# Kernel optimization log

Measured on AMD Instinct MI355X. Metric: run time of the kernel, lower is better.

Reference implementation:

```python
import jax, jax.numpy as jnp
import numpy as np

B, CIN, H, W = 16, 3, 112, 112
S, D, C, NC = 3, 4, 128, 100   # num_scales, depth, channels, num_classes
THRESH = 0.9
WSCALE = 0.05  # keep activations numerically sane through relu-conv cascade


def _conv3x3(x, w, b):
    # x: [B,Cin,H,W], w: [Cout,Cin,3,3]
    y = jax.lax.conv_general_dilated(
        x, w, window_strides=(1, 1), padding='SAME',
        dimension_numbers=('NCHW', 'OIHW', 'NCHW'))
    return y + b[None, :, None, None]


def setup_inputs() -> dict:
    key = jax.random.key(0)
    k = jax.random.split(key, 7)
    return {
        'x': jax.random.normal(k[0], (B, CIN, H, W), jnp.float32),
        'init_w': jax.random.normal(k[1], (S, C, CIN, 3, 3), jnp.float32) * WSCALE,
        'init_b': jax.random.normal(k[2], (S, C), jnp.float32) * WSCALE,
        'block_w': jax.random.normal(k[3], (D, S, C, C, 3, 3), jnp.float32) * WSCALE,
        'block_b': jax.random.normal(k[4], (D, S, C), jnp.float32) * WSCALE,
        'cls_w': jax.random.normal(k[5], (D, NC, C), jnp.float32) * WSCALE,
        'cls_b': jax.random.normal(k[6], (D, NC), jnp.float32) * WSCALE,
    }


def reference(x, init_w, init_b, block_w, block_b, cls_w, cls_b):
    # init blocks: one conv per scale (no activation, as in source)
    feats = [_conv3x3(x, init_w[s], init_b[s]) for s in range(S)]

    outputs = jnp.zeros((x.shape[0], cls_w.shape[1]), x.dtype)
    exited = jnp.zeros((x.shape[0],), jnp.bool_)

    # exit_layers = [0..D-1], so classifier index == block index
    for i in range(D):
        feats = [jax.nn.relu(_conv3x3(feats[s], block_w[i, s], block_b[i, s]))
                 for s in range(S)]
        pooled = feats[-1].mean(axis=(2, 3))              # [B, C]
        logits = pooled @ cls_w[i].T + cls_b[i]           # [B, NC]
        conf = jnp.max(jax.nn.softmax(logits, axis=-1), axis=-1)
        take = jnp.logical_and(~exited, conf >= THRESH)   # vectorized early-exit
        outputs = jnp.where(take[:, None], logits, outputs)
        exited = jnp.logical_or(exited, take)

    # samples that never exited get the last classifier's logits
    final_logits = feats[-1].mean(axis=(2, 3)) @ cls_w[-1].T + cls_b[-1]
    outputs = jnp.where(exited[:, None], outputs, final_logits)
    return outputs
```

## Files before the change

### kernel.cpp

```cpp
#include <hip/hip_runtime.h>
#include <hip/hip_bf16.h>


typedef unsigned int uint;
typedef unsigned short u16;
typedef __bf16 bf16x8 __attribute__((ext_vector_type(8)));
typedef short short8 __attribute__((ext_vector_type(8)));
typedef unsigned short ushort8 __attribute__((ext_vector_type(8)));
typedef float f32x4 __attribute__((ext_vector_type(4)));

#define NB   16
#define CCH  128
#define NCLS 100
#define HW   12544
#define NTILE 98

__device__ __forceinline__ u16 f2bf(float f) {
    uint u = __float_as_uint(f);
    return (u16)((u + 0x7fffu + ((u >> 16) & 1u)) >> 16);
}

__device__ __forceinline__ void gload16(const u16* g, u16* l) {
    __builtin_amdgcn_global_load_lds(
        (const __attribute__((address_space(1))) uint*)g,
        (__attribute__((address_space(3))) uint*)l, 16, 0, 0);
}

__global__ __launch_bounds__(256) void convert_w(
    const float* __restrict__ bw, u16* __restrict__ wbs)
{
    int idx = blockIdx.x * 256 + threadIdx.x;
    if (idx >= 4 * 147456) return;
    int d = idx / 147456, r = idx % 147456;
    int s = r >> 12;
    int p = r & 4095;
    int co = p >> 5, gpos = (p >> 3) & 3, e = p & 7;
    int q = s / 9, t = s % 9;
    int cin = q * 32 + ((gpos ^ ((co >> 1) & 3)) << 3) + e;
    float v = bw[(((size_t)(d * 3 + 2) * 128 + co) * 128 + cin) * 9 + t];
    wbs[idx] = f2bf(v);
}

__global__ __launch_bounds__(256) void conv_init(
    const float* __restrict__ in,
    const float* __restrict__ wgt,
    const float* __restrict__ bias,
    u16* __restrict__ outp)
{
    const int tile = blockIdx.x;
    const int cg   = blockIdx.y;
    const int n    = blockIdx.z;
    const int h0 = (tile / 7) * 16, w0 = (tile % 7) * 16;
    const int tid = threadIdx.x;
    const int sid = tid & 63, wv = tid >> 6;
    const int tx = sid & 7, ty = sid >> 3;

    __shared__ float s_in[3][18][18];
    __shared__ float s_w[3][9][32];

    float acc[2][2][8];
    #pragma unroll
    for (int a = 0; a < 2; a++)
        #pragma unroll
        for (int b = 0; b < 2; b++)
            #pragma unroll
            for (int c = 0; c < 8; c++) acc[a][b][c] = 0.f;

    const float* in_n = in + (size_t)n * 3 * HW;
    const int cbase = cg * 32;

    for (int e = tid; e < 3 * 324; e += 256) {
        int ck = e / 324, p = e % 324;
        int y = p / 18, x = p % 18;
        int gh = h0 + y - 1, gw = w0 + x - 1;
        float v = 0.f;
        if ((unsigned)gh < 112u && (unsigned)gw < 112u)
            v = in_n[(size_t)ck * HW + gh * 112 + gw];
        s_in[ck][y][x] = v;
    }
    for (int e = tid; e < 3 * 9 * 32; e += 256) {
        int co = e / 27, r = e % 27;
        int ck = r / 9, kidx = r % 9;
        s_w[ck][kidx][co] = wgt[((size_t)(cbase + co) * 3 + ck) * 9 + kidx];
    }
    __syncthreads();

    #pragma unroll
    for (int ck = 0; ck < 3; ck++) {
        float rowv[4][4];
        #pragma unroll
        for (int r = 0; r < 4; r++) {
            float2 a  = *(const float2*)&s_in[ck][ty * 2 + r][tx * 2];
            float2 b2 = *(const float2*)&s_in[ck][ty * 2 + r][tx * 2 + 2];
            rowv[r][0] = a.x; rowv[r][1] = a.y;
            rowv[r][2] = b2.x; rowv[r][3] = b2.y;
        }
        #pragma unroll
        for (int kh = 0; kh < 3; kh++)
            #pragma unroll
            for (int kw = 0; kw < 3; kw++) {
                float i00 = rowv[kh][kw],     i01 = rowv[kh][kw + 1];
                float i10 = rowv[kh + 1][kw], i11 = rowv[kh + 1][kw + 1];
                const float* wp = &s_w[ck][kh * 3 + kw][wv * 8];
                #pragma unroll
                for (int co = 0; co < 8; co++) {
                    float wval = wp[co];
                    acc[0][0][co] += i00 * wval;
                    acc[0][1][co] += i01 * wval;
                    acc[1][0][co] += i10 * wval;
                    acc[1][1][co] += i11 * wval;
                }
            }
    }

    float bv[8];
    #pragma unroll
    for (int co = 0; co < 8; co++) bv[co] = bias[cbase + wv * 8 + co];
    #pragma unroll
    for (int dy = 0; dy < 2; dy++)
        #pragma unroll
        for (int dx = 0; dx < 2; dx++) {
            ushort8 pk;
            #pragma unroll
            for (int co = 0; co < 8; co++)
                pk[co] = f2bf(acc[dy][dx][co] + bv[co]);
            int h = h0 + ty * 2 + dy, w = w0 + tx * 2 + dx;
            *(ushort8*)(outp + (((size_t)n * HW + h * 112 + w) << 7) + cbase + wv * 8) = pk;
        }
}

#define AS 40

template<bool STORE>
__global__ __launch_bounds__(256, 3) void conv_mfma(
    const u16* __restrict__ in,
    const u16* __restrict__ wbs,
    const float* __restrict__ bias,
    u16* __restrict__ outp,
    float* __restrict__ partial)
{
    __shared__ u16 s_in[180 * AS];
    __shared__ u16 s_w[4][4096];
    float* s_pool = (float*)s_in;

    const int tile = blockIdx.x;
    const int n    = blockIdx.y;
    const int h0 = (tile / 7) * 8, w0 = (tile % 7) * 16;
    const int tid = threadIdx.x, lane = tid & 63;
    const int wid = tid >> 6, wm = wid >> 1, wn = wid & 1;
    const int l15 = lane & 15, l4 = lane >> 4;

    const u16* in_n = in + ((size_t)n * HW << 7);

    const u16* wsrc_base = wbs + wid * 1024 + (lane << 3);
    u16* wdst_base = &s_w[0][0] + wid * 1024;

    #pragma unroll
    for (int s01 = 0; s01 < 2; ++s01) {
        const u16* src = wsrc_base + (s01 << 12);
        u16* dst = wdst_base + (s01 << 12);
        gload16(src, dst);
        gload16(src + 512, dst + 512);
    }

    #pragma unroll
    for (int r2 = 0; r2 < 3; ++r2) {
        int g = tid + (r2 << 8);
        if (g < 720) {
            int px = g >> 2, c8 = (g & 3) << 3;
            int hh = px / 18, ww2 = px - hh * 18;
            int gh = h0 + hh - 1, gw = w0 + ww2 - 1;
            uint4 v = make_uint4(0, 0, 0, 0);
            if ((unsigned)gh < 112u && (unsigned)gw < 112u)
                v = *(const uint4*)(in_n + ((size_t)(gh * 112 + gw) << 7) + c8);
            *(uint4*)(s_in + px * AS + c8) = v;
        }
    }

    f32x4 acc[4][4];
    #pragma unroll
    for (int i = 0; i < 4; ++i)
        #pragma unroll
        for (int j = 0; j < 4; ++j)
            #pragma unroll
            for (int e = 0; e < 4; ++e) acc[i][j][e] = 0.f;

    int a_base[4], b_base[4];
    #pragma unroll
    for (int fi = 0; fi < 4; ++fi) a_base[fi] = (wm * 4 + fi) * 18 + l15;
    #pragma unroll
    for (int nj = 0; nj < 4; ++nj)
        b_base[nj] = (wn * 64 + nj * 16 + l15) * 32 + ((l4 ^ ((l15 >> 1) & 3)) << 3);

    __syncthreads();

    #pragma unroll
    for (int P = 0; P < 18; ++P) {
        const int s0 = 2 * P, s1 = 2 * P + 1;

        #pragma unroll
        for (int d2 = 2; d2 < 4; ++d2) {
            const int sp = s0 + d2;
            if (sp < 36) {
                const u16* src = wsrc_base + (sp << 12);
                u16* dst = wdst_base + ((sp & 3) << 12);
                gload16(src, dst);
                gload16(src + 512, dst + 512);
            }
        }

        {
            const int t = s0 % 9, kh = t / 3, kw = t - kh * 3;
            bf16x8 a[4], b[4];
            #pragma unroll
            for (int fi = 0; fi < 4; ++fi) {
                const u16* p = s_in + (a_base[fi] + kh * 18 + kw) * AS + (l4 << 3);
                a[fi] = __builtin_bit_cast(bf16x8, *(const short8*)p);
            }
            const u16* rb = &s_w[s0 & 3][0];
            #pragma unroll
            for (int nj = 0; nj < 4; ++nj)
                b[nj] = __builtin_bit_cast(bf16x8, *(const short8*)(rb + b_base[nj]));
            #pragma unroll
            for (int fi = 0; fi < 4; ++fi)
                #pragma unroll
                for (int nj = 0; nj < 4; ++nj)
                    acc[fi][nj] = __builtin_amdgcn_mfma_f32_16x16x32_bf16(
                        a[fi], b[nj], acc[fi][nj], 0, 0, 0);
        }

        if (s0 % 9 == 8) {
            const int qn = s0 / 9 + 1;
            asm volatile("s_waitcnt lgkmcnt(0)" ::: "memory");
            __builtin_amdgcn_s_barrier();
            #pragma unroll
            for (int r2 = 0; r2 < 3; ++r2) {
                int g = tid + (r2 << 8);
                if (g < 720) {
                    int px = g >> 2, c8 = (g & 3) << 3;
                    int hh = px / 18, ww2 = px - hh * 18;
                    int gh = h0 + hh - 1, gw = w0 + ww2 - 1;
                    uint4 v = make_uint4(0, 0, 0, 0);
                    if ((unsigned)gh < 112u && (unsigned)gw < 112u)
                        v = *(const uint4*)(in_n + ((size_t)(gh * 112 + gw) << 7)
                                            + (qn << 5) + c8);
                    *(uint4*)(s_in + px * AS + c8) = v;
                }
            }
            asm volatile("s_waitcnt lgkmcnt(0)" ::: "memory");
            __builtin_amdgcn_s_barrier();
            __builtin_amdgcn_sched_barrier(0);
        }

        {
            const int t = s1 % 9, kh = t / 3, kw = t - kh * 3;
            bf16x8 a[4], b[4];
            #pragma unroll
            for (int fi = 0; fi < 4; ++fi) {
                const u16* p = s_in + (a_base[fi] + kh * 18 + kw) * AS + (l4 << 3);
                a[fi] = __builtin_bit_cast(bf16x8, *(const short8*)p);
            }
            const u16* rb = &s_w[s1 & 3][0];
            #pragma unroll
            for (int nj = 0; nj < 4; ++nj)
                b[nj] = __builtin_bit_cast(bf16x8, *(const short8*)(rb + b_base[nj]));
            #pragma unroll
            for (int fi = 0; fi < 4; ++fi)
                #pragma unroll
                for (int nj = 0; nj < 4; ++nj)
                    acc[fi][nj] = __builtin_amdgcn_mfma_f32_16x16x32_bf16(
                        a[fi], b[nj], acc[fi][nj], 0, 0, 0);
        }

        asm volatile("s_waitcnt vmcnt(0)" ::: "memory");
        __builtin_amdgcn_s_barrier();
        __builtin_amdgcn_sched_barrier(0);

        if (s1 % 9 == 8 && s1 != 35) {
            const int qn = s1 / 9 + 1;
            #pragma unroll
            for (int r2 = 0; r2 < 3; ++r2) {
                int g = tid + (r2 << 8);
                if (g < 720) {
                    int px = g >> 2, c8 = (g & 3) << 3;
                    int hh = px / 18, ww2 = px - hh * 18;
                    int gh = h0 + hh - 1, gw = w0 + ww2 - 1;
                    uint4 v = make_uint4(0, 0, 0, 0);
                    if ((unsigned)gh < 112u && (unsigned)gw < 112u)
                        v = *(const uint4*)(in_n + ((size_t)(gh * 112 + gw) << 7)
                                            + (qn << 5) + c8);
                    *(uint4*)(s_in + px * AS + c8) = v;
                }
            }
            asm volatile("s_waitcnt lgkmcnt(0)" ::: "memory");
            __builtin_amdgcn_s_barrier();
            __builtin_amdgcn_sched_barrier(0);
        }
    }

    float bv[4], ps[4];
    #pragma unroll
    for (int nj = 0; nj < 4; ++nj) { bv[nj] = bias[wn * 64 + nj * 16 + l15]; ps[nj] = 0.f; }
    u16* out_n = outp + ((size_t)n * HW << 7);
    #pragma unroll
    for (int fi = 0; fi < 4; ++fi) {
        int h = h0 + wm * 4 + fi;
        #pragma unroll
        for (int j = 0; j < 4; ++j) {
            int w = w0 + (l4 << 2) + j;
            u16* pr = out_n + ((size_t)(h * 112 + w) << 7);
            #pragma unroll
            for (int nj = 0; nj < 4; ++nj) {
                float v = fmaxf(acc[fi][nj][j] + bv[nj], 0.f);
                ps[nj] += v;
                if (STORE) pr[wn * 64 + nj * 16 + l15] = f2bf(v);
            }
        }
    }
    #pragma unroll
    for (int nj = 0; nj < 4; ++nj) {
        ps[nj] += __shfl_xor(ps[nj], 16, 64);
        ps[nj] += __shfl_xor(ps[nj], 32, 64);
    }
    __syncthreads();
    if (l4 == 0) {
        #pragma unroll
        for (int nj = 0; nj < 4; ++nj)
            s_pool[wm * 128 + wn * 64 + nj * 16 + l15] = ps[nj];
    }
    __syncthreads();
    if (tid < 128)
        partial[((size_t)n * NTILE + tile) * 128 + tid] = s_pool[tid] + s_pool[128 + tid];
}

__global__ __launch_bounds__(128) void logits_k(
    const float* __restrict__ partial,
    const float* __restrict__ cw,
    const float* __restrict__ cb,
    float* __restrict__ lg)
{
    const int i = blockIdx.x, n = blockIdx.y;
    const int tid = threadIdx.x;
    __shared__ float pool[128];
    const float* pp = partial + ((size_t)(i * NB + n) * NTILE) * 128;
    float s = 0.f;
    for (int t = 0; t < NTILE; ++t) s += pp[t * 128 + tid];
    pool[tid] = s * (1.f / HW);
    __syncthreads();
    if (tid < NCLS) {
        const float* wp = cw + ((size_t)i * NCLS + tid) * CCH;
        float a = cb[i * NCLS + tid];
        #pragma unroll
        for (int c = 0; c < CCH; c += 4) {
            float4 w4 = *(const float4*)(wp + c);
            a += pool[c] * w4.x + pool[c + 1] * w4.y
               + pool[c + 2] * w4.z + pool[c + 3] * w4.w;
        }
        lg[(i * NB + n) * NCLS + tid] = a;
    }
}

__global__ __launch_bounds__(256) void select_k(
    const float* __restrict__ lg,
    float* __restrict__ out)
{
    __shared__ float slg[4 * NB * NCLS];
    __shared__ int chosen[NB];
    const int tid = threadIdx.x;
    for (int e = tid; e < 4 * NB * NCLS; e += 256) slg[e] = lg[e];
    __syncthreads();
    if (tid < NB) {
        int n = tid, ch = 3;
        for (int i = 0; i < 3; i++) {
            const float* row = &slg[(i * NB + n) * NCLS];
            float m = -1e30f;
            for (int j = 0; j < NCLS; j++) m = fmaxf(m, row[j]);
            float se = 0.f;
            for (int j = 0; j < NCLS; j++) se += expf(row[j] - m);
            if (1.f / se >= 0.9f) { ch = i; break; }
        }
        chosen[n] = ch;
    }
    __syncthreads();
    for (int e = tid; e < NB * NCLS; e += 256) {
        int n = e / NCLS, j = e % NCLS;
        out[e] = slg[(chosen[n] * NB + n) * NCLS + j];
    }
}

extern "C" void kernel_launch(void* const* d_in, const int* in_sizes, int n_in,
                              void* d_out, int out_size, void* d_ws, size_t ws_size,
                              hipStream_t stream) {
    const float* x       = (const float*)d_in[0];
    const float* init_w  = (const float*)d_in[1];
    const float* init_b  = (const float*)d_in[2];
    const float* block_w = (const float*)d_in[3];
    const float* block_b = (const float*)d_in[4];
    const float* cls_w   = (const float*)d_in[5];
    const float* cls_b   = (const float*)d_in[6];
    float* out = (float*)d_out;

    char* ws = (char*)d_ws;
    u16* fA        = (u16*)ws;
    u16* fB        = (u16*)(ws + 51380224);
    u16* wbs       = (u16*)(ws + 102760448);
    float* partial = (float*)(ws + 103940096);
    float* lgbuf   = (float*)(ws + 107151360);

    convert_w<<<2304, 256, 0, stream>>>(block_w, wbs);
    conv_init<<<dim3(49, 4, NB), 256, 0, stream>>>(
        x, init_w + 2 * 128 * 27, init_b + 2 * 128, fA);

    u16* cur = fA;
    u16* nxt = fB;
    for (int i = 0; i < 4; ++i) {
        if (i < 3)
            conv_mfma<true><<<dim3(NTILE, NB), 256, 0, stream>>>(
                cur, wbs + (size_t)i * 147456, block_b + (i * 3 + 2) * 128, nxt,
                partial + (size_t)i * NB * NTILE * 128);
        else
            conv_mfma<false><<<dim3(NTILE, NB), 256, 0, stream>>>(
                cur, wbs + (size_t)i * 147456, block_b + (i * 3 + 2) * 128, nxt,
                partial + (size_t)i * NB * NTILE * 128);
        u16* t = cur; cur = nxt; nxt = t;
    }

    logits_k<<<dim3(4, NB), 128, 0, stream>>>(partial, cls_w, cls_b, lgbuf);
    select_k<<<1, 256, 0, stream>>>(lgbuf, out);
}
```

Before: 315.6 us.

## Switch weight staging to a 3-buffer ring with per-step barriers and 4 blocks/CU

Replaces the 4-slot weight ring, which was processed two K-steps per barrier, with a 3-slot ring processed one step at a time. It waits with vmcnt(2) so the prefetch two steps ahead stays in flight. The smaller LDS footprint lets launch bounds request 4 resident blocks per CU instead of 3, raising occupancy so other blocks can hide latency. The cost is twice as many barriers per block and possible register pressure from the tighter bound.

Result: faster. 297.9 us (-5.6%).

```diff
diff --git a/kernel.cpp b/kernel.cpp
--- a/kernel.cpp
+++ b/kernel.cpp
@@ -132,7 +132,7 @@
 #define AS 40
 
 template<bool STORE>
-__global__ __launch_bounds__(256, 3) void conv_mfma(
+__global__ __launch_bounds__(256, 4) void conv_mfma(
     const u16* __restrict__ in,
     const u16* __restrict__ wbs,
     const float* __restrict__ bias,
@@ -140,7 +140,7 @@
     float* __restrict__ partial)
 {
     __shared__ u16 s_in[180 * AS];
-    __shared__ u16 s_w[4][4096];
+    __shared__ u16 s_w[3][4096];
     float* s_pool = (float*)s_in;
 
     const int tile = blockIdx.x;
@@ -195,44 +195,43 @@
     __syncthreads();
 
     #pragma unroll
-    for (int P = 0; P < 18; ++P) {
-        const int s0 = 2 * P, s1 = 2 * P + 1;
-
-        #pragma unroll
-        for (int d2 = 2; d2 < 4; ++d2) {
-            const int sp = s0 + d2;
-            if (sp < 36) {
-                const u16* src = wsrc_base + (sp << 12);
-                u16* dst = wdst_base + ((sp & 3) << 12);
-                gload16(src, dst);
-                gload16(src + 512, dst + 512);
-            }
-        }
-
-        {
-            const int t = s0 % 9, kh = t / 3, kw = t - kh * 3;
-            bf16x8 a[4], b[4];
-            #pragma unroll
-            for (int fi = 0; fi < 4; ++fi) {
-                const u16* p = s_in + (a_base[fi] + kh * 18 + kw) * AS + (l4 << 3);
-                a[fi] = __builtin_bit_cast(bf16x8, *(const short8*)p);
-            }
-            const u16* rb = &s_w[s0 & 3][0];
+    for (int s = 0; s < 36; ++s) {
+        if (s + 2 < 36) {
+            const u16* src = wsrc_base + ((s + 2) << 12);
+            u16* dst = wdst_base + (((s + 2) % 3) << 12);
+            gload16(src, dst);
+            gload16(src + 512, dst + 512);
+        }
+
+        const int t = s % 9, kh = t / 3, kw = t - kh * 3;
+        bf16x8 a[4], b[4];
+        #pragma unroll
+        for (int fi = 0; fi < 4; ++fi) {
+            const u16* p = s_in + (a_base[fi] + kh * 18 + kw) * AS + (l4 << 3);
+            a[fi] = __builtin_bit_cast(bf16x8, *(const short8*)p);
+        }
+        const u16* rb = &s_w[s % 3][0];
+        #pragma unroll
+        for (int nj = 0; nj < 4; ++nj)
+            b[nj] = __builtin_bit_cast(bf16x8, *(const short8*)(rb + b_base[nj]));
+
+        #pragma unroll
+        for (int fi = 0; fi < 4; ++fi)
             #pragma unroll
             for (int nj = 0; nj < 4; ++nj)
-                b[nj] = __builtin_bit_cast(bf16x8, *(const short8*)(rb + b_base[nj]));
-            #pragma unroll
-            for (int fi = 0; fi < 4; ++fi)
-                #pragma unroll
-                for (int nj = 0; nj < 4; ++nj)
-                    acc[fi][nj] = __builtin_amdgcn_mfma_f32_16x16x32_bf16(
-                        a[fi], b[nj], acc[fi][nj], 0, 0, 0);
-        }
-
-        if (s0 % 9 == 8) {
-            const int qn = s0 / 9 + 1;
+                acc[fi][nj] = __builtin_amdgcn_mfma_f32_16x16x32_bf16(
+                    a[fi], b[nj], acc[fi][nj], 0, 0, 0);
+
+        if (s < 35) {
+            if (s + 2 < 36) asm volatile("s_waitcnt vmcnt(2)" ::: "memory");
+            else            asm volatile("s_waitcnt vmcnt(0)" ::: "memory");
             asm volatile("s_waitcnt lgkmcnt(0)" ::: "memory");
             __builtin_amdgcn_s_barrier();
+            __builtin_amdgcn_sched_barrier(0);
+        }
+
+        if (t == 8 && s < 35) {
+            const int qn = s / 9 + 1;
             #pragma unroll
             for (int r2 = 0; r2 < 3; ++r2) {
                 int g = tid + (r2 << 8);
@@ -251,51 +250,6 @@
             __builtin_amdgcn_s_barrier();
             __builtin_amdgcn_sched_barrier(0);
         }
-
-        {
-            const int t = s1 % 9, kh = t / 3, kw = t - kh * 3;
-            bf16x8 a[4], b[4];
-            #pragma unroll
-            for (int fi = 0; fi < 4; ++fi) {
-                const u16* p = s_in + (a_base[fi] + kh * 18 + kw) * AS + (l4 << 3);
-                a[fi] = __builtin_bit_cast(bf16x8, *(const short8*)p);
-            }
-            const u16* rb = &s_w[s1 & 3][0];
-            #pragma unroll
-            for (int nj = 0; nj < 4; ++nj)
-                b[nj] = __builtin_bit_cast(bf16x8, *(const short8*)(rb + b_base[nj]));
-            #pragma unroll
-            for (int fi = 0; fi < 4; ++fi)
-                #pragma unroll
-                for (int nj = 0; nj < 4; ++nj)
-                    acc[fi][nj] = __builtin_amdgcn_mfma_f32_16x16x32_bf16(
-                        a[fi], b[nj], acc[fi][nj], 0, 0, 0);
-        }
-
-        asm volatile("s_waitcnt vmcnt(0)" ::: "memory");
-        __builtin_amdgcn_s_barrier();
-        __builtin_amdgcn_sched_barrier(0);
-
-        if (s1 % 9 == 8 && s1 != 35) {
-            const int qn = s1 / 9 + 1;
-            #pragma unroll
-            for (int r2 = 0; r2 < 3; ++r2) {
-                int g = tid + (r2 << 8);
-                if (g < 720) {
-                    int px = g >> 2, c8 = (g & 3) << 3;
-                    int hh = px / 18, ww2 = px - hh * 18;
-                    int gh = h0 + hh - 1, gw = w0 + ww2 - 1;
-                    uint4 v = make_uint4(0, 0, 0, 0);
-                    if ((unsigned)gh < 112u && (unsigned)gw < 112u)
-                        v = *(const uint4*)(in_n + ((size_t)(gh * 112 + gw) << 7)
-                                            + (qn << 5) + c8);
-                    *(uint4*)(s_in + px * AS + c8) = v;
-                }
-            }
-            asm volatile("s_waitcnt lgkmcnt(0)" ::: "memory");
-            __builtin_amdgcn_s_barrier();
-            __builtin_amdgcn_sched_barrier(0);
-        }
     }
 
     float bv[4], ps[4];
```
